# Optimization experiments

Hardware: AMD Instinct MI355X
Metric: run time of the kernel (lower is better)

## Reference

```python
import jax, jax.numpy as jnp
import numpy as np

# --- config (Qwen3-Next linear attention defaults) ---
B, S, H = 1, 256, 2048
NK, NV, DK, DV, K = 4, 32, 128, 128, 4
KEY_DIM = NK * DK          # 512
VAL_DIM = NV * DV          # 4096
CONV_DIM = 2 * KEY_DIM + VAL_DIM  # 5120
EPS = 1e-6


def setup_inputs() -> dict:
    key = jax.random.key(0)
    ks = jax.random.split(key, 8)
    rn = lambda k, shape, sc: jax.random.normal(k, shape, jnp.float32) * sc
    return {
        "hidden_states": jax.random.normal(ks[0], (B, S, H), jnp.float32),
        "w_qkvz": rn(ks[1], (2 * KEY_DIM + 2 * VAL_DIM, H), 0.02),  # in_proj_qkvz weight
        "w_ba": rn(ks[2], (2 * NV, H), 0.02),                        # in_proj_ba weight
        "w_out": rn(ks[3], (H, VAL_DIM), 0.02),                      # out_proj weight
        "conv_w": rn(ks[4], (CONV_DIM, 1, K), 0.1),                  # depthwise conv weight [C,1,K]
        "dt_bias": jnp.ones((NV,), jnp.float32),
        "A_log": jnp.zeros((NV,), jnp.float32),
        "norm_w": jnp.ones((DV,), jnp.float32),
    }


def reference(hidden_states, w_qkvz, w_ba, w_out, conv_w, dt_bias, A_log, norm_w):
    b, s, _ = hidden_states.shape
    # input projections (Linear without bias: x @ W.T)
    qkvz = hidden_states @ w_qkvz.T                      # [B,S,9216]
    ba = hidden_states @ w_ba.T                          # [B,S,64]
    q, k, v, z = jnp.split(qkvz, [KEY_DIM, 2 * KEY_DIM, 2 * KEY_DIM + VAL_DIM], axis=-1)
    beta, alpha = jnp.split(ba, 2, axis=-1)              # each [B,S,NV]

    # causal depthwise conv over concat(q,k,v), then silu
    qkv = jnp.concatenate([q, k, v], axis=-1).transpose(0, 2, 1)   # [B,C,S]
    qkv = jax.lax.conv_general_dilated(
        qkv, conv_w, window_strides=(1,), padding=[(K - 1, 0)],
        dimension_numbers=("NCH", "OIH", "NCH"), feature_group_count=CONV_DIM)
    qkv = jax.nn.silu(qkv).transpose(0, 2, 1)            # [B,S,C]
    q, k, v = jnp.split(qkv, [KEY_DIM, 2 * KEY_DIM], axis=-1)

    q = q.reshape(b, s, NK, DK)
    k = k.reshape(b, s, NK, DK)
    v = v.reshape(b, s, NV, DV)
    z = z.reshape(b, s, NV, DV)

    # GQA-style head expansion (repeat_interleave)
    ratio = NV // NK
    q = jnp.repeat(q, ratio, axis=2)                     # [B,S,NV,DK]
    k = jnp.repeat(k, ratio, axis=2)

    # NOTE: original computes g = -softplus(-A_log - alpha) but never uses it (dead code).
    beta_g = jax.nn.sigmoid(beta + dt_bias)[..., None]   # [B,S,NV,1]
    q = q * (DK ** -0.5)

    # naive delta-rule: full outer-product tensor + cumsum (memory-bound)
    kv = jnp.einsum("bsnk,bsnv->bsnkv", k, v * beta_g)   # [B,S,NV,DK,DV]
    out = jnp.einsum("bsnk,bsnkv->bsnv", q, jnp.cumsum(kv, axis=1))  # [B,S,NV,DV]

    # gated RMSNorm over head_v_dim in fp32
    of = out.astype(jnp.float32)
    var = jnp.mean(of * of, axis=-1, keepdims=True)
    of = of * jax.lax.rsqrt(var + EPS) * norm_w
    of = of * jax.nn.silu(z.astype(jnp.float32))

    return of.reshape(b, s, VAL_DIM) @ w_out.T           # [B,S,H]
```

## Files before the change

### kernel.cpp

```cpp
#include <hip/hip_runtime.h>
#include <hip/hip_bf16.h>

#define S_LEN   256
#define HID     2048
#define NVH     32
#define DKD     128
#define DVD     128
#define KEYDIM  512
#define VALDIM  4096
#define CONVDIM 5120
#define QKVZ_N  9216
#define EPS_F   1e-6f

typedef __attribute__((ext_vector_type(8))) short bf16x8;
typedef __attribute__((ext_vector_type(4))) float f32x4;

__device__ __forceinline__ unsigned short f2bf(float f) {
    union { float f; unsigned int i; } v; v.f = f;
    unsigned int x = v.i;
    return (unsigned short)((x + 0x7FFFu + ((x >> 16) & 1u)) >> 16);
}
__device__ __forceinline__ unsigned int pk2(float x, float y) {
    union { __hip_bfloat162 h; unsigned int u; } c;
    c.h = __float22bfloat162_rn(float2{x, y});
    return c.u;
}
__device__ __forceinline__ void gl_lds16(const void* g, void* l) {
    __builtin_amdgcn_global_load_lds(
        (const __attribute__((address_space(1))) unsigned int*)g,
        (__attribute__((address_space(3))) unsigned int*)l,
        16, 0, 0);
}

template<int NT>
__global__ __launch_bounds__(256, 3)
void gemm_db(const unsigned short* __restrict__ A, const float* __restrict__ B,
             float* __restrict__ Cpart, int N, int K, int kc) {
    __shared__ __align__(16) unsigned short As[2][128][64];
    __shared__ __align__(16) unsigned short Bs[2][NT][64];

    const int tid  = threadIdx.x;
    const int lane = tid & 63, wave = tid >> 6;
    const int wm = wave >> 1, wn = wave & 1;
    const int quad = lane >> 4, l16 = lane & 15;
    const int m0 = (blockIdx.x & 1) * 128;
    const int n0 = (blockIdx.x >> 1) * NT;
    const int kbeg = blockIdx.y * kc;
    const int niter = kc >> 6;

    const int a_ro = lane >> 3;
    const int a_gc = (lane & 7) ^ a_ro;

    const int rB = tid >> 2;
    const int cB = (tid & 3) * 16;
    const int swB = rB & 7;

    f32x4 acc[4][2];
#pragma unroll
    for (int i = 0; i < 4; i++)
#pragma unroll
        for (int j = 0; j < 2; j++) acc[i][j] = (f32x4){0.f, 0.f, 0.f, 0.f};

    float4 br[4];
    auto ldB = [&](int kk) {
        const float* p = B + (size_t)(n0 + rB) * K + kk + cB;
        br[0] = *(const float4*)(p);
        br[1] = *(const float4*)(p + 4);
        br[2] = *(const float4*)(p + 8);
        br[3] = *(const float4*)(p + 12);
    };
    auto wrB = [&](int buf) {
        uint4 u0, u1;
        u0.x = pk2(br[0].x, br[0].y); u0.y = pk2(br[0].z, br[0].w);
        u0.z = pk2(br[1].x, br[1].y); u0.w = pk2(br[1].z, br[1].w);
        u1.x = pk2(br[2].x, br[2].y); u1.y = pk2(br[2].z, br[2].w);
        u1.z = pk2(br[3].x, br[3].y); u1.w = pk2(br[3].z, br[3].w);
        int c0 = ((tid & 3) * 2) ^ swB;
        int c1 = ((tid & 3) * 2 + 1) ^ swB;
        *(uint4*)(&Bs[buf][rB][c0 * 8]) = u0;
        *(uint4*)(&Bs[buf][rB][c1 * 8]) = u1;
    };
    auto stageA = [&](int buf, int kk) {
#pragma unroll
        for (int t = 0; t < 4; ++t) {
            int rbase = wave * 32 + t * 8;
            gl_lds16(A + (size_t)(m0 + rbase + a_ro) * K + kk + a_gc * 8,
                     &As[buf][rbase][0]);
        }
    };
    auto compute = [&](int buf) {
#pragma unroll
        for (int ks = 0; ks < 2; ++ks) {
            bf16x8 af[4], bfr[2];
            int c = ((ks * 4 + quad) ^ (l16 & 7)) * 8;
#pragma unroll
            for (int i = 0; i < 4; ++i)
                af[i] = *(const bf16x8*)(&As[buf][wm * 64 + i * 16 + l16][c]);
#pragma unroll
            for (int j = 0; j < 2; ++j)
                bfr[j] = *(const bf16x8*)(&Bs[buf][wn * 32 + j * 16 + l16][c]);
#pragma unroll
            for (int i = 0; i < 4; ++i)
#pragma unroll
                for (int j = 0; j < 2; ++j)
                    acc[i][j] = __builtin_amdgcn_mfma_f32_16x16x32_bf16(af[i], bfr[j], acc[i][j], 0, 0, 0);
        }
    };

    ldB(kbeg);
    stageA(0, kbeg);
    wrB(0);
    if (niter > 1) ldB(kbeg + 64);
    __syncthreads();

    for (int it = 0; it < niter; ++it) {
        if (it + 1 < niter) stageA((it + 1) & 1, kbeg + (it + 1) * 64);
        compute(it & 1);
        if (it + 1 < niter) wrB((it + 1) & 1);
        if (it + 2 < niter) ldB(kbeg + (it + 2) * 64);
        __syncthreads();
    }

    float* C = Cpart + (size_t)blockIdx.y * 256 * N;
#pragma unroll
    for (int i = 0; i < 4; i++)
#pragma unroll
        for (int j = 0; j < 2; j++)
#pragma unroll
            for (int r = 0; r < 4; r++) {
                int row = m0 + wm * 64 + i * 16 + quad * 4 + r;
                int col = n0 + wn * 32 + j * 16 + l16;
                C[(size_t)row * N + col] = acc[i][j][r];
            }
}

template<int P>
__global__ void reduce_sum(const float* __restrict__ part, float* __restrict__ out, int n) {
    int i = (blockIdx.x * 256 + threadIdx.x) * 4;
    if (i >= n) return;
    float4 s = *(const float4*)(part + i);
#pragma unroll
    for (int p = 1; p < P; p++) {
        float4 v = *(const float4*)(part + (size_t)p * n + i);
        s.x += v.x; s.y += v.y; s.z += v.z; s.w += v.w;
    }
    *(float4*)(out + i) = s;
}

__global__ __launch_bounds__(256)
void ba_proj_cvt(const float* __restrict__ hs, const float* __restrict__ w_ba,
                 float* __restrict__ ba, unsigned short* __restrict__ abf) {
    int s = blockIdx.x;
    int n = threadIdx.x & 63, seg = threadIdx.x >> 6;
    const float* x = hs + (size_t)s * HID + seg * 512;
    const float* w = w_ba + (size_t)n * HID + seg * 512;
    float acc = 0.f;
#pragma unroll 4
    for (int k = 0; k < 512; k += 4) {
        float4 xv = *(const float4*)(x + k);
        float4 wv = *(const float4*)(w + k);
        acc += xv.x * wv.x + xv.y * wv.y + xv.z * wv.z + xv.w * wv.w;
    }
    __shared__ float parts[4][64];
    parts[seg][n] = acc;
    {
        int d = threadIdx.x * 8;
        const float4* p = (const float4*)(hs + (size_t)s * HID + d);
        float4 a = p[0], b = p[1];
        uint4 r;
        r.x = pk2(a.x, a.y); r.y = pk2(a.z, a.w);
        r.z = pk2(b.x, b.y); r.w = pk2(b.z, b.w);
        *(uint4*)(abf + (size_t)s * HID + d) = r;
    }
    __syncthreads();
    if (threadIdx.x < 64)
        ba[s * 64 + threadIdx.x] = parts[0][threadIdx.x] + parts[1][threadIdx.x]
                                 + parts[2][threadIdx.x] + parts[3][threadIdx.x];
}

template<int P>
__global__ __launch_bounds__(256)
void sum_conv(const float* __restrict__ part, const float* __restrict__ conv_w,
              float* __restrict__ conv, float* __restrict__ zs) {
    const int s0 = blockIdx.y * 8;
    const int c  = blockIdx.x * 1024 + threadIdx.x * 4;
    auto sum4 = [&](int s) {
        const float* p = part + (size_t)s * QKVZ_N + c;
        float4 v = *(const float4*)p;
#pragma unroll
        for (int q = 1; q < P; q++) {
            float4 w = *(const float4*)(p + (size_t)q * S_LEN * QKVZ_N);
            v.x += w.x; v.y += w.y; v.z += w.z; v.w += w.w;
        }
        return v;
    };
    if (c < CONVDIM) {
        float4 cw[4];
#pragma unroll
        for (int i = 0; i < 4; ++i) cw[i] = *(const float4*)(conv_w + (size_t)(c + i) * 4);
        float4 w0{0,0,0,0}, w1{0,0,0,0}, w2{0,0,0,0};
        for (int s = (s0 >= 3 ? s0 - 3 : 0); s < s0; ++s) { w0 = w1; w1 = w2; w2 = sum4(s); }
        for (int s = s0; s < s0 + 8; ++s) {
            float4 w3 = sum4(s);
            float4 o;
            o.x = w0.x * cw[0].x + w1.x * cw[0].y + w2.x * cw[0].z + w3.x * cw[0].w;
            o.y = w0.y * cw[1].x + w1.y * cw[1].y + w2.y * cw[1].z + w3.y * cw[1].w;
            o.z = w0.z * cw[2].x + w1.z * cw[2].y + w2.z * cw[2].z + w3.z * cw[2].w;
            o.w = w0.w * cw[3].x + w1.w * cw[3].y + w2.w * cw[3].z + w3.w * cw[3].w;
            o.x = o.x / (1.f + __expf(-o.x));
            o.y = o.y / (1.f + __expf(-o.y));
            o.z = o.z / (1.f + __expf(-o.z));
            o.w = o.w / (1.f + __expf(-o.w));
            *(float4*)(conv + (size_t)s * CONVDIM + c) = o;
            w0 = w1; w1 = w2; w2 = w3;
        }
    } else {
        for (int s = s0; s < s0 + 8; ++s) {
            float4 v = sum4(s);
            *(float4*)(zs + (size_t)s * VALDIM + (c - CONVDIM)) = v;
        }
    }
}

__global__ __launch_bounds__(256)
void scores_k(const float* __restrict__ conv, const float* __restrict__ ba,
              const float* __restrict__ dt_bias, float* __restrict__ scores) {
    int p = blockIdx.x;
    int st = (int)((__fsqrt_rn(8.f * p + 1.f) - 1.f) * 0.5f);
    while ((st + 1) * (st + 2) / 2 <= p) st++;
    while (st * (st + 1) / 2 > p) st--;
    int tt = p - st * (st + 1) / 2;
    int hk = blockIdx.y;
    int s0 = st * 16, t0 = tt * 16;
    __shared__ float Qs[16][132], Ks[16][132];
    int tid = threadIdx.x;
    int qoff = hk * DKD;
    int koff = KEYDIM + hk * DKD;
    for (int idx = tid; idx < 16 * 128; idx += 256) {
        int i = idx >> 7, d = idx & 127;
        Qs[i][d] = conv[(size_t)(s0 + i) * CONVDIM + qoff + d];
        Ks[i][d] = conv[(size_t)(t0 + i) * CONVDIM + koff + d];
    }
    __syncthreads();
    int tx = tid & 15, ty = tid >> 4;
    int s = s0 + ty, t = t0 + tx;
    float dot = 0.f;
    for (int d = 0; d < 128; d++) dot += Qs[ty][d] * Ks[tx][d];
    float base = (t <= s) ? dot * 0.08838834764831845f : 0.f;
#pragma unroll
    for (int v = 0; v < 8; v++) {
        int n = hk * 8 + v;
        float b = ba[t * 64 + n] + dt_bias[n];
        float bg = 1.f / (1.f + __expf(-b));
        scores[((size_t)n * 256 + s) * 256 + t] = base * bg;
    }
}

__global__ __launch_bounds__(256)
void attn_rms(const float* __restrict__ scores, const float* __restrict__ conv,
              const float* __restrict__ zs, const float* __restrict__ norm_w,
              unsigned short* __restrict__ normed) {
    int n = blockIdx.y, s0 = blockIdx.x * 16;
    int voff = 2 * KEYDIM + n * DVD;
    __shared__ float Ss[16][17];
    __shared__ float Vs[16][132];
    int tid = threadIdx.x, sy = tid >> 4, dx = tid & 15;
    float acc[8] = {0.f, 0.f, 0.f, 0.f, 0.f, 0.f, 0.f, 0.f};
    for (int t0 = 0; t0 <= s0; t0 += 16) {
        Ss[sy][dx] = scores[((size_t)n * 256 + s0 + sy) * 256 + t0 + dx];
        const float* vp = conv + (size_t)(t0 + sy) * CONVDIM + voff + dx * 8;
        *(float4*)&Vs[sy][dx * 8]     = *(const float4*)vp;
        *(float4*)&Vs[sy][dx * 8 + 4] = *(const float4*)(vp + 4);
        __syncthreads();
#pragma unroll
        for (int j = 0; j < 16; j++) {
            float sv = Ss[sy][j];
#pragma unroll
            for (int r = 0; r < 8; r++) acc[r] += sv * Vs[j][dx + 16 * r];
        }
        __syncthreads();
    }
    float ssq = 0.f;
#pragma unroll
    for (int r = 0; r < 8; r++) ssq += acc[r] * acc[r];
#pragma unroll
    for (int m = 1; m <= 8; m <<= 1) ssq += __shfl_xor(ssq, m, 64);
    float inv = rsqrtf(ssq * (1.f / 128.f) + EPS_F);
    int s = s0 + sy;
#pragma unroll
    for (int r = 0; r < 8; r++) {
        int d = dx + 16 * r;
        float z = zs[(size_t)s * VALDIM + n * DVD + d];
        float sz = z / (1.f + __expf(-z));
        float v = acc[r] * inv * norm_w[d] * sz;
        normed[((size_t)s * NVH + n) * DVD + d] = f2bf(v);
    }
}

extern "C" void kernel_launch(void* const* d_in, const int* in_sizes, int n_in,
                              void* d_out, int out_size, void* d_ws, size_t ws_size,
                              hipStream_t stream) {
    const float* hs      = (const float*)d_in[0];
    const float* w_qkvz  = (const float*)d_in[1];
    const float* w_ba    = (const float*)d_in[2];
    const float* w_out   = (const float*)d_in[3];
    const float* conv_w  = (const float*)d_in[4];
    const float* dt_bias = (const float*)d_in[5];
    const float* norm_w  = (const float*)d_in[7];

    char* ws = (char*)d_ws;
    unsigned short* abf = (unsigned short*)ws; ws += (size_t)S_LEN * HID * 2;
    float* ba   = (float*)ws;  ws += (size_t)S_LEN * 64 * 4;
    float* conv = (float*)ws;  ws += (size_t)S_LEN * CONVDIM * 4;
    float* zs   = (float*)ws;  ws += (size_t)S_LEN * VALDIM * 4;
    char* regB = ws;
    const bool big = ws_size >= (size_t)50 * 1024 * 1024;
    const int sk1 = big ? 4 : 2;
    const int sk2 = big ? 8 : 4;
    float* scratch1 = (float*)regB;
    unsigned short* normed = (unsigned short*)regB;
    float* scratch2 = (float*)(regB + 2097152);
    float* scores   = (float*)(regB + 2097152 + (size_t)sk2 * 2097152);

    ba_proj_cvt<<<S_LEN, 256, 0, stream>>>(hs, w_ba, ba, abf);
    gemm_db<64><<<dim3(2 * (QKVZ_N / 64), sk1), 256, 0, stream>>>(abf, w_qkvz, scratch1, QKVZ_N, HID, HID / sk1);
    if (big) sum_conv<4><<<dim3(9, 32), 256, 0, stream>>>(scratch1, conv_w, conv, zs);
    else     sum_conv<2><<<dim3(9, 32), 256, 0, stream>>>(scratch1, conv_w, conv, zs);
    scores_k<<<dim3(136, 4), 256, 0, stream>>>(conv, ba, dt_bias, scores);
    attn_rms<<<dim3(16, NVH), 256, 0, stream>>>(scores, conv, zs, norm_w, normed);
    gemm_db<64><<<dim3(2 * (HID / 64), sk2), 256, 0, stream>>>(normed, w_out, scratch2, HID, VALDIM, VALDIM / sk2);
    if (big) reduce_sum<8><<<(S_LEN * HID) / 1024, 256, 0, stream>>>(scratch2, (float*)d_out, S_LEN * HID);
    else     reduce_sum<4><<<(S_LEN * HID) / 1024, 256, 0, stream>>>(scratch2, (float*)d_out, S_LEN * HID);
}
```

Before: 247.0 us.

## Triple-buffer A in GEMM, drop split-K for QKVZ projection, read z directly

The GEMM now keeps A tiles in a three-stage LDS ring with two register sets for B, prefetching two iterations ahead. It uses a lighter barrier that waits only on LDS counters, with occupancy lowered from 3 to 2 blocks. The QKVZ projection no longer splits K, so the partial-sum reduction in the conv kernel and the separate z buffer go away; attn_rms reads z straight from the qkvz output. The out-projection split-K is fixed at 4 regardless of workspace size. This may under-fill the GPU for the first GEMM (288 blocks) in exchange for less memory traffic, and the barrier no longer waits on vmcnt, which relies on the global_load_lds ordering being correct.

```diff
diff --git a/kernel.cpp b/kernel.cpp
--- a/kernel.cpp
+++ b/kernel.cpp
@@ -31,12 +31,19 @@
         (__attribute__((address_space(3))) unsigned int*)l,
         16, 0, 0);
 }
+__device__ __forceinline__ void pipe_barrier() {
+    __builtin_amdgcn_sched_barrier(0);
+    asm volatile("s_waitcnt lgkmcnt(0)" ::: "memory");
+    __builtin_amdgcn_s_barrier();
+    asm volatile("" ::: "memory");
+    __builtin_amdgcn_sched_barrier(0);
+}
 
 template<int NT>
-__global__ __launch_bounds__(256, 3)
+__global__ __launch_bounds__(256, 2)
 void gemm_db(const unsigned short* __restrict__ A, const float* __restrict__ B,
              float* __restrict__ Cpart, int N, int K, int kc) {
-    __shared__ __align__(16) unsigned short As[2][128][64];
+    __shared__ __align__(16) unsigned short As[3][128][64];
     __shared__ __align__(16) unsigned short Bs[2][NT][64];
 
     const int tid  = threadIdx.x;
@@ -50,7 +57,6 @@
 
     const int a_ro = lane >> 3;
     const int a_gc = (lane & 7) ^ a_ro;
-
     const int rB = tid >> 2;
     const int cB = (tid & 3) * 16;
     const int swB = rB & 7;
@@ -61,15 +67,16 @@
 #pragma unroll
         for (int j = 0; j < 2; j++) acc[i][j] = (f32x4){0.f, 0.f, 0.f, 0.f};
 
-    float4 br[4];
-    auto ldB = [&](int kk) {
+    float4 brA[4], brB[4];
+
+    auto ldB = [&](float4 (&br)[4], int kk) {
         const float* p = B + (size_t)(n0 + rB) * K + kk + cB;
         br[0] = *(const float4*)(p);
         br[1] = *(const float4*)(p + 4);
         br[2] = *(const float4*)(p + 8);
         br[3] = *(const float4*)(p + 12);
     };
-    auto wrB = [&](int buf) {
+    auto wrB = [&](int bb, float4 (&br)[4]) {
         uint4 u0, u1;
         u0.x = pk2(br[0].x, br[0].y); u0.y = pk2(br[0].z, br[0].w);
         u0.z = pk2(br[1].x, br[1].y); u0.w = pk2(br[1].z, br[1].w);
@@ -77,28 +84,28 @@
         u1.z = pk2(br[3].x, br[3].y); u1.w = pk2(br[3].z, br[3].w);
         int c0 = ((tid & 3) * 2) ^ swB;
         int c1 = ((tid & 3) * 2 + 1) ^ swB;
-        *(uint4*)(&Bs[buf][rB][c0 * 8]) = u0;
-        *(uint4*)(&Bs[buf][rB][c1 * 8]) = u1;
-    };
-    auto stageA = [&](int buf, int kk) {
+        *(uint4*)(&Bs[bb][rB][c0 * 8]) = u0;
+        *(uint4*)(&Bs[bb][rB][c1 * 8]) = u1;
+    };
+    auto stageA = [&](int ab, int kk) {
 #pragma unroll
         for (int t = 0; t < 4; ++t) {
             int rbase = wave * 32 + t * 8;
             gl_lds16(A + (size_t)(m0 + rbase + a_ro) * K + kk + a_gc * 8,
-                     &As[buf][rbase][0]);
+                     &As[ab][rbase][0]);
         }
     };
-    auto compute = [&](int buf) {
+    auto compute = [&](int ab, int bb) {
 #pragma unroll
         for (int ks = 0; ks < 2; ++ks) {
             bf16x8 af[4], bfr[2];
             int c = ((ks * 4 + quad) ^ (l16 & 7)) * 8;
 #pragma unroll
             for (int i = 0; i < 4; ++i)
-                af[i] = *(const bf16x8*)(&As[buf][wm * 64 + i * 16 + l16][c]);
+                af[i] = *(const bf16x8*)(&As[ab][wm * 64 + i * 16 + l16][c]);
 #pragma unroll
             for (int j = 0; j < 2; ++j)
-                bfr[j] = *(const bf16x8*)(&Bs[buf][wn * 32 + j * 16 + l16][c]);
+                bfr[j] = *(const bf16x8*)(&Bs[bb][wn * 32 + j * 16 + l16][c]);
 #pragma unroll
             for (int i = 0; i < 4; ++i)
 #pragma unroll
@@ -107,18 +114,27 @@
         }
     };
 
-    ldB(kbeg);
+    auto step = [&](int it, float4 (&brLoad)[4], float4 (&brCons)[4]) {
+        if (it + 2 < niter) {
+            int kn = kbeg + (it + 2) * 64;
+            stageA((it + 2) % 3, kn);
+            ldB(brLoad, kn);
+        }
+        if (it + 1 < niter) wrB((it + 1) & 1, brCons);
+        compute(it % 3, it & 1);
+        pipe_barrier();
+    };
+
     stageA(0, kbeg);
-    wrB(0);
-    if (niter > 1) ldB(kbeg + 64);
-    __syncthreads();
-
-    for (int it = 0; it < niter; ++it) {
-        if (it + 1 < niter) stageA((it + 1) & 1, kbeg + (it + 1) * 64);
-        compute(it & 1);
-        if (it + 1 < niter) wrB((it + 1) & 1);
-        if (it + 2 < niter) ldB(kbeg + (it + 2) * 64);
-        __syncthreads();
+    ldB(brA, kbeg);
+    if (niter > 1) { stageA(1, kbeg + 64); ldB(brB, kbeg + 64); }
+    wrB(0, brA);
+    pipe_barrier();
+
+    int it = 0;
+    while (true) {
+        step(it, brA, brB); ++it; if (it >= niter) break;
+        step(it, brB, brA); ++it; if (it >= niter) break;
     }
 
     float* C = Cpart + (size_t)blockIdx.y * 256 * N;
@@ -178,47 +194,30 @@
                                  + parts[2][threadIdx.x] + parts[3][threadIdx.x];
 }
 
-template<int P>
 __global__ __launch_bounds__(256)
-void sum_conv(const float* __restrict__ part, const float* __restrict__ conv_w,
-              float* __restrict__ conv, float* __restrict__ zs) {
+void conv_silu4(const float* __restrict__ qkvz, const float* __restrict__ conv_w,
+                float* __restrict__ conv) {
     const int s0 = blockIdx.y * 8;
     const int c  = blockIdx.x * 1024 + threadIdx.x * 4;
-    auto sum4 = [&](int s) {
-        const float* p = part + (size_t)s * QKVZ_N + c;
-        float4 v = *(const float4*)p;
-#pragma unroll
-        for (int q = 1; q < P; q++) {
-            float4 w = *(const float4*)(p + (size_t)q * S_LEN * QKVZ_N);
-            v.x += w.x; v.y += w.y; v.z += w.z; v.w += w.w;
-        }
-        return v;
-    };
-    if (c < CONVDIM) {
-        float4 cw[4];
-#pragma unroll
-        for (int i = 0; i < 4; ++i) cw[i] = *(const float4*)(conv_w + (size_t)(c + i) * 4);
-        float4 w0{0,0,0,0}, w1{0,0,0,0}, w2{0,0,0,0};
-        for (int s = (s0 >= 3 ? s0 - 3 : 0); s < s0; ++s) { w0 = w1; w1 = w2; w2 = sum4(s); }
-        for (int s = s0; s < s0 + 8; ++s) {
-            float4 w3 = sum4(s);
-            float4 o;
-            o.x = w0.x * cw[0].x + w1.x * cw[0].y + w2.x * cw[0].z + w3.x * cw[0].w;
-            o.y = w0.y * cw[1].x + w1.y * cw[1].y + w2.y * cw[1].z + w3.y * cw[1].w;
-            o.z = w0.z * cw[2].x + w1.z * cw[2].y + w2.z * cw[2].z + w3.z * cw[2].w;
-            o.w = w0.w * cw[3].x + w1.w * cw[3].y + w2.w * cw[3].z + w3.w * cw[3].w;
-            o.x = o.x / (1.f + __expf(-o.x));
-            o.y = o.y / (1.f + __expf(-o.y));
-            o.z = o.z / (1.f + __expf(-o.z));
-            o.w = o.w / (1.f + __expf(-o.w));
-            *(float4*)(conv + (size_t)s * CONVDIM + c) = o;
-            w0 = w1; w1 = w2; w2 = w3;
-        }
-    } else {
-        for (int s = s0; s < s0 + 8; ++s) {
-            float4 v = sum4(s);
-            *(float4*)(zs + (size_t)s * VALDIM + (c - CONVDIM)) = v;
-        }
+    auto rd4 = [&](int s) { return *(const float4*)(qkvz + (size_t)s * QKVZ_N + c); };
+    float4 cw[4];
+#pragma unroll
+    for (int i = 0; i < 4; ++i) cw[i] = *(const float4*)(conv_w + (size_t)(c + i) * 4);
+    float4 w0{0,0,0,0}, w1{0,0,0,0}, w2{0,0,0,0};
+    for (int s = (s0 >= 3 ? s0 - 3 : 0); s < s0; ++s) { w0 = w1; w1 = w2; w2 = rd4(s); }
+    for (int s = s0; s < s0 + 8; ++s) {
+        float4 w3 = rd4(s);
+        float4 o;
+        o.x = w0.x * cw[0].x + w1.x * cw[0].y + w2.x * cw[0].z + w3.x * cw[0].w;
+        o.y = w0.y * cw[1].x + w1.y * cw[1].y + w2.y * cw[1].z + w3.y * cw[1].w;
+        o.z = w0.z * cw[2].x + w1.z * cw[2].y + w2.z * cw[2].z + w3.z * cw[2].w;
+        o.w = w0.w * cw[3].x + w1.w * cw[3].y + w2.w * cw[3].z + w3.w * cw[3].w;
+        o.x = o.x / (1.f + __expf(-o.x));
+        o.y = o.y / (1.f + __expf(-o.y));
+        o.z = o.z / (1.f + __expf(-o.z));
+        o.w = o.w / (1.f + __expf(-o.w));
+        *(float4*)(conv + (size_t)s * CONVDIM + c) = o;
+        w0 = w1; w1 = w2; w2 = w3;
     }
 }
 
@@ -258,7 +257,7 @@
 
 __global__ __launch_bounds__(256)
 void attn_rms(const float* __restrict__ scores, const float* __restrict__ conv,
-              const float* __restrict__ zs, const float* __restrict__ norm_w,
+              const float* __restrict__ qkvz, const float* __restrict__ norm_w,
               unsigned short* __restrict__ normed) {
     int n = blockIdx.y, s0 = blockIdx.x * 16;
     int voff = 2 * KEYDIM + n * DVD;
@@ -290,7 +289,7 @@
 #pragma unroll
     for (int r = 0; r < 8; r++) {
         int d = dx + 16 * r;
-        float z = zs[(size_t)s * VALDIM + n * DVD + d];
+        float z = qkvz[(size_t)s * QKVZ_N + CONVDIM + n * DVD + d];
         float sz = z / (1.f + __expf(-z));
         float v = acc[r] * inv * norm_w[d] * sz;
         normed[((size_t)s * NVH + n) * DVD + d] = f2bf(v);
@@ -310,25 +309,18 @@
 
     char* ws = (char*)d_ws;
     unsigned short* abf = (unsigned short*)ws; ws += (size_t)S_LEN * HID * 2;
-    float* ba   = (float*)ws;  ws += (size_t)S_LEN * 64 * 4;
-    float* conv = (float*)ws;  ws += (size_t)S_LEN * CONVDIM * 4;
-    float* zs   = (float*)ws;  ws += (size_t)S_LEN * VALDIM * 4;
-    char* regB = ws;
-    const bool big = ws_size >= (size_t)50 * 1024 * 1024;
-    const int sk1 = big ? 4 : 2;
-    const int sk2 = big ? 8 : 4;
-    float* scratch1 = (float*)regB;
-    unsigned short* normed = (unsigned short*)regB;
-    float* scratch2 = (float*)(regB + 2097152);
-    float* scores   = (float*)(regB + 2097152 + (size_t)sk2 * 2097152);
+    float* ba     = (float*)ws;  ws += (size_t)S_LEN * 64 * 4;
+    float* qkvz   = (float*)ws;  ws += (size_t)S_LEN * QKVZ_N * 4;
+    float* conv   = (float*)ws;  ws += (size_t)S_LEN * CONVDIM * 4;
+    unsigned short* normed = (unsigned short*)ws; ws += (size_t)S_LEN * VALDIM * 2;
+    float* scores = (float*)ws;  ws += (size_t)NVH * S_LEN * S_LEN * 4;
+    float* scratch2 = (float*)ws;
 
     ba_proj_cvt<<<S_LEN, 256, 0, stream>>>(hs, w_ba, ba, abf);
-    gemm_db<64><<<dim3(2 * (QKVZ_N / 64), sk1), 256, 0, stream>>>(abf, w_qkvz, scratch1, QKVZ_N, HID, HID / sk1);
-    if (big) sum_conv<4><<<dim3(9, 32), 256, 0, stream>>>(scratch1, conv_w, conv, zs);
-    else     sum_conv<2><<<dim3(9, 32), 256, 0, stream>>>(scratch1, conv_w, conv, zs);
+    gemm_db<64><<<dim3(2 * (QKVZ_N / 64), 1), 256, 0, stream>>>(abf, w_qkvz, qkvz, QKVZ_N, HID, HID);
+    conv_silu4<<<dim3(5, 32), 256, 0, stream>>>(qkvz, conv_w, conv);
     scores_k<<<dim3(136, 4), 256, 0, stream>>>(conv, ba, dt_bias, scores);
-    attn_rms<<<dim3(16, NVH), 256, 0, stream>>>(scores, conv, zs, norm_w, normed);
-    gemm_db<64><<<dim3(2 * (HID / 64), sk2), 256, 0, stream>>>(normed, w_out, scratch2, HID, VALDIM, VALDIM / sk2);
-    if (big) reduce_sum<8><<<(S_LEN * HID) / 1024, 256, 0, stream>>>(scratch2, (float*)d_out, S_LEN * HID);
-    else     reduce_sum<4><<<(S_LEN * HID) / 1024, 256, 0, stream>>>(scratch2, (float*)d_out, S_LEN * HID);
-}
+    attn_rms<<<dim3(16, NVH), 256, 0, stream>>>(scores, conv, qkvz, norm_w, normed);
+    gemm_db<64><<<dim3(2 * (HID / 64), 4), 256, 0, stream>>>(normed, w_out, scratch2, HID, VALDIM, VALDIM / 4);
+    reduce_sum<4><<<(S_LEN * HID) / 1024, 256, 0, stream>>>(scratch2, (float*)d_out, S_LEN * HID);
+}
```

Result: slower. 267.7 us (+8.4%).

## Deepen GEMM pipeline with triple-buffered A and ping-pong B register prefetch

Applied to the files above, without the earlier changes.

The bf16 GEMM kernel now keeps three LDS stages for A, filled by global_load_lds, and alternates two register sets for the fp32 B tiles. This gives a prefetch distance of two iterations, and the loop is manually unrolled to swap the register sets. The plain __syncthreads is replaced by a custom barrier with sched_barrier fences that waits only on lgkmcnt, so global loads stay in flight across the barrier. The aim is to hide global-memory latency better. In exchange, LDS use and register pressure rise and launch bounds drop from 3 to 2 waves per EU, and correctness depends on the compiler placing vmcnt waits correctly.

```diff
diff --git a/kernel.cpp b/kernel.cpp
--- a/kernel.cpp
+++ b/kernel.cpp
@@ -31,12 +31,19 @@
         (__attribute__((address_space(3))) unsigned int*)l,
         16, 0, 0);
 }
+__device__ __forceinline__ void pipe_barrier() {
+    __builtin_amdgcn_sched_barrier(0);
+    asm volatile("s_waitcnt lgkmcnt(0)" ::: "memory");
+    __builtin_amdgcn_s_barrier();
+    asm volatile("" ::: "memory");
+    __builtin_amdgcn_sched_barrier(0);
+}
 
 template<int NT>
-__global__ __launch_bounds__(256, 3)
+__global__ __launch_bounds__(256, 2)
 void gemm_db(const unsigned short* __restrict__ A, const float* __restrict__ B,
              float* __restrict__ Cpart, int N, int K, int kc) {
-    __shared__ __align__(16) unsigned short As[2][128][64];
+    __shared__ __align__(16) unsigned short As[3][128][64];
     __shared__ __align__(16) unsigned short Bs[2][NT][64];
 
     const int tid  = threadIdx.x;
@@ -50,7 +57,6 @@
 
     const int a_ro = lane >> 3;
     const int a_gc = (lane & 7) ^ a_ro;
-
     const int rB = tid >> 2;
     const int cB = (tid & 3) * 16;
     const int swB = rB & 7;
@@ -61,15 +67,16 @@
 #pragma unroll
         for (int j = 0; j < 2; j++) acc[i][j] = (f32x4){0.f, 0.f, 0.f, 0.f};
 
-    float4 br[4];
-    auto ldB = [&](int kk) {
+    float4 brA[4], brB[4];
+
+    auto ldB = [&](float4 (&br)[4], int kk) {
         const float* p = B + (size_t)(n0 + rB) * K + kk + cB;
         br[0] = *(const float4*)(p);
         br[1] = *(const float4*)(p + 4);
         br[2] = *(const float4*)(p + 8);
         br[3] = *(const float4*)(p + 12);
     };
-    auto wrB = [&](int buf) {
+    auto wrB = [&](int bb, float4 (&br)[4]) {
         uint4 u0, u1;
         u0.x = pk2(br[0].x, br[0].y); u0.y = pk2(br[0].z, br[0].w);
         u0.z = pk2(br[1].x, br[1].y); u0.w = pk2(br[1].z, br[1].w);
@@ -77,28 +84,28 @@
         u1.z = pk2(br[3].x, br[3].y); u1.w = pk2(br[3].z, br[3].w);
         int c0 = ((tid & 3) * 2) ^ swB;
         int c1 = ((tid & 3) * 2 + 1) ^ swB;
-        *(uint4*)(&Bs[buf][rB][c0 * 8]) = u0;
-        *(uint4*)(&Bs[buf][rB][c1 * 8]) = u1;
-    };
-    auto stageA = [&](int buf, int kk) {
+        *(uint4*)(&Bs[bb][rB][c0 * 8]) = u0;
+        *(uint4*)(&Bs[bb][rB][c1 * 8]) = u1;
+    };
+    auto stageA = [&](int ab, int kk) {
 #pragma unroll
         for (int t = 0; t < 4; ++t) {
             int rbase = wave * 32 + t * 8;
             gl_lds16(A + (size_t)(m0 + rbase + a_ro) * K + kk + a_gc * 8,
-                     &As[buf][rbase][0]);
-        }
-    };
-    auto compute = [&](int buf) {
+                     &As[ab][rbase][0]);
+        }
+    };
+    auto compute = [&](int ab, int bb) {
 #pragma unroll
         for (int ks = 0; ks < 2; ++ks) {
             bf16x8 af[4], bfr[2];
             int c = ((ks * 4 + quad) ^ (l16 & 7)) * 8;
 #pragma unroll
             for (int i = 0; i < 4; ++i)
-                af[i] = *(const bf16x8*)(&As[buf][wm * 64 + i * 16 + l16][c]);
+                af[i] = *(const bf16x8*)(&As[ab][wm * 64 + i * 16 + l16][c]);
 #pragma unroll
             for (int j = 0; j < 2; ++j)
-                bfr[j] = *(const bf16x8*)(&Bs[buf][wn * 32 + j * 16 + l16][c]);
+                bfr[j] = *(const bf16x8*)(&Bs[bb][wn * 32 + j * 16 + l16][c]);
 #pragma unroll
             for (int i = 0; i < 4; ++i)
 #pragma unroll
@@ -107,18 +114,27 @@
         }
     };
 
-    ldB(kbeg);
+    auto step = [&](int it, float4 (&brLoad)[4], float4 (&brCons)[4]) {
+        if (it + 2 < niter) {
+            int kn = kbeg + (it + 2) * 64;
+            stageA((it + 2) % 3, kn);
+            ldB(brLoad, kn);
+        }
+        if (it + 1 < niter) wrB((it + 1) & 1, brCons);
+        compute(it % 3, it & 1);
+        pipe_barrier();
+    };
+
     stageA(0, kbeg);
-    wrB(0);
-    if (niter > 1) ldB(kbeg + 64);
-    __syncthreads();
-
-    for (int it = 0; it < niter; ++it) {
-        if (it + 1 < niter) stageA((it + 1) & 1, kbeg + (it + 1) * 64);
-        compute(it & 1);
-        if (it + 1 < niter) wrB((it + 1) & 1);
-        if (it + 2 < niter) ldB(kbeg + (it + 2) * 64);
-        __syncthreads();
+    ldB(brA, kbeg);
+    if (niter > 1) { stageA(1, kbeg + 64); ldB(brB, kbeg + 64); }
+    wrB(0, brA);
+    pipe_barrier();
+
+    int it = 0;
+    while (true) {
+        step(it, brA, brB); ++it; if (it >= niter) break;
+        step(it, brB, brA); ++it; if (it >= niter) break;
     }
 
     float* C = Cpart + (size_t)blockIdx.y * 256 * N;
```

After: 260.7 us. +5.6%, slower.

## Replace LDS double-buffered GEMM with register-streaming GEMM and deeper split-K

Applied to the files above, without the earlier changes.

The shared-memory double-buffered GEMM is replaced by a kernel where each wave owns 16 output columns across all 256 rows. It streams fp32 weights straight into registers, converts them to bf16 and reads A fragments directly from global memory, with no LDS staging and no barriers. Split-K for the output projection goes up to 16/8 partitions, with a matching reduction and a higher workspace threshold. This targets the weight-bandwidth-bound GEMMs with a small M. The trade-off is heavy uncached A re-reads, more accumulator registers, and extra partial-sum traffic.

```diff
diff --git a/kernel.cpp b/kernel.cpp
--- a/kernel.cpp
+++ b/kernel.cpp
@@ -25,113 +25,48 @@
     c.h = __float22bfloat162_rn(float2{x, y});
     return c.u;
 }
-__device__ __forceinline__ void gl_lds16(const void* g, void* l) {
-    __builtin_amdgcn_global_load_lds(
-        (const __attribute__((address_space(1))) unsigned int*)g,
-        (__attribute__((address_space(3))) unsigned int*)l,
-        16, 0, 0);
-}
-
-template<int NT>
-__global__ __launch_bounds__(256, 3)
-void gemm_db(const unsigned short* __restrict__ A, const float* __restrict__ B,
-             float* __restrict__ Cpart, int N, int K, int kc) {
-    __shared__ __align__(16) unsigned short As[2][128][64];
-    __shared__ __align__(16) unsigned short Bs[2][NT][64];
-
+__device__ __forceinline__ bf16x8 pack_bf8(float4 lo, float4 hi) {
+    union { uint4 u; bf16x8 h; } c;
+    c.u.x = pk2(lo.x, lo.y); c.u.y = pk2(lo.z, lo.w);
+    c.u.z = pk2(hi.x, hi.y); c.u.w = pk2(hi.z, hi.w);
+    return c.h;
+}
+
+template<int KC>
+__global__ __launch_bounds__(256, 2)
+void gemm_stream(const unsigned short* __restrict__ A, const float* __restrict__ B,
+                 float* __restrict__ Cpart, int N, int K) {
     const int tid  = threadIdx.x;
     const int lane = tid & 63, wave = tid >> 6;
-    const int wm = wave >> 1, wn = wave & 1;
-    const int quad = lane >> 4, l16 = lane & 15;
-    const int m0 = (blockIdx.x & 1) * 128;
-    const int n0 = (blockIdx.x >> 1) * NT;
-    const int kbeg = blockIdx.y * kc;
-    const int niter = kc >> 6;
-
-    const int a_ro = lane >> 3;
-    const int a_gc = (lane & 7) ^ a_ro;
-
-    const int rB = tid >> 2;
-    const int cB = (tid & 3) * 16;
-    const int swB = rB & 7;
-
-    f32x4 acc[4][2];
-#pragma unroll
-    for (int i = 0; i < 4; i++)
-#pragma unroll
-        for (int j = 0; j < 2; j++) acc[i][j] = (f32x4){0.f, 0.f, 0.f, 0.f};
-
-    float4 br[4];
-    auto ldB = [&](int kk) {
-        const float* p = B + (size_t)(n0 + rB) * K + kk + cB;
-        br[0] = *(const float4*)(p);
-        br[1] = *(const float4*)(p + 4);
-        br[2] = *(const float4*)(p + 8);
-        br[3] = *(const float4*)(p + 12);
-    };
-    auto wrB = [&](int buf) {
-        uint4 u0, u1;
-        u0.x = pk2(br[0].x, br[0].y); u0.y = pk2(br[0].z, br[0].w);
-        u0.z = pk2(br[1].x, br[1].y); u0.w = pk2(br[1].z, br[1].w);
-        u1.x = pk2(br[2].x, br[2].y); u1.y = pk2(br[2].z, br[2].w);
-        u1.z = pk2(br[3].x, br[3].y); u1.w = pk2(br[3].z, br[3].w);
-        int c0 = ((tid & 3) * 2) ^ swB;
-        int c1 = ((tid & 3) * 2 + 1) ^ swB;
-        *(uint4*)(&Bs[buf][rB][c0 * 8]) = u0;
-        *(uint4*)(&Bs[buf][rB][c1 * 8]) = u1;
-    };
-    auto stageA = [&](int buf, int kk) {
-#pragma unroll
-        for (int t = 0; t < 4; ++t) {
-            int rbase = wave * 32 + t * 8;
-            gl_lds16(A + (size_t)(m0 + rbase + a_ro) * K + kk + a_gc * 8,
-                     &As[buf][rbase][0]);
-        }
-    };
-    auto compute = [&](int buf) {
-#pragma unroll
-        for (int ks = 0; ks < 2; ++ks) {
-            bf16x8 af[4], bfr[2];
-            int c = ((ks * 4 + quad) ^ (l16 & 7)) * 8;
-#pragma unroll
-            for (int i = 0; i < 4; ++i)
-                af[i] = *(const bf16x8*)(&As[buf][wm * 64 + i * 16 + l16][c]);
-#pragma unroll
-            for (int j = 0; j < 2; ++j)
-                bfr[j] = *(const bf16x8*)(&Bs[buf][wn * 32 + j * 16 + l16][c]);
-#pragma unroll
-            for (int i = 0; i < 4; ++i)
-#pragma unroll
-                for (int j = 0; j < 2; ++j)
-                    acc[i][j] = __builtin_amdgcn_mfma_f32_16x16x32_bf16(af[i], bfr[j], acc[i][j], 0, 0, 0);
-        }
-    };
-
-    ldB(kbeg);
-    stageA(0, kbeg);
-    wrB(0);
-    if (niter > 1) ldB(kbeg + 64);
-    __syncthreads();
-
-    for (int it = 0; it < niter; ++it) {
-        if (it + 1 < niter) stageA((it + 1) & 1, kbeg + (it + 1) * 64);
-        compute(it & 1);
-        if (it + 1 < niter) wrB((it + 1) & 1);
-        if (it + 2 < niter) ldB(kbeg + (it + 2) * 64);
-        __syncthreads();
-    }
-
-    float* C = Cpart + (size_t)blockIdx.y * 256 * N;
-#pragma unroll
-    for (int i = 0; i < 4; i++)
-#pragma unroll
-        for (int j = 0; j < 2; j++)
-#pragma unroll
-            for (int r = 0; r < 4; r++) {
-                int row = m0 + wm * 64 + i * 16 + quad * 4 + r;
-                int col = n0 + wn * 32 + j * 16 + l16;
-                C[(size_t)row * N + col] = acc[i][j][r];
-            }
+    const int l16 = lane & 15, quad = lane >> 4;
+    const int n0 = blockIdx.x * 64 + wave * 16;
+    const int kbeg = blockIdx.y * KC;
+
+    const unsigned short* a0 = A + (size_t)l16 * K + kbeg + quad * 8;
+    const float*          b0 = B + (size_t)(n0 + l16) * K + kbeg + quad * 8;
+
+    f32x4 acc[16];
+#pragma unroll
+    for (int i = 0; i < 16; i++) acc[i] = (f32x4){0.f, 0.f, 0.f, 0.f};
+
+#pragma unroll 4
+    for (int ks = 0; ks < KC; ks += 32) {
+        float4 x = *(const float4*)(b0 + ks);
+        float4 y = *(const float4*)(b0 + ks + 4);
+        bf16x8 bf = pack_bf8(x, y);
+#pragma unroll
+        for (int i = 0; i < 16; i++) {
+            bf16x8 af = *(const bf16x8*)(a0 + (size_t)i * 16 * K + ks);
+            acc[i] = __builtin_amdgcn_mfma_f32_16x16x32_bf16(af, bf, acc[i], 0, 0, 0);
+        }
+    }
+
+    float* C = Cpart + (size_t)blockIdx.y * 256 * N + n0 + l16;
+#pragma unroll
+    for (int i = 0; i < 16; i++)
+#pragma unroll
+        for (int r = 0; r < 4; r++)
+            C[(size_t)(i * 16 + quad * 4 + r) * N] = acc[i][r];
 }
 
 template<int P>
@@ -314,21 +249,23 @@
     float* conv = (float*)ws;  ws += (size_t)S_LEN * CONVDIM * 4;
     float* zs   = (float*)ws;  ws += (size_t)S_LEN * VALDIM * 4;
     char* regB = ws;
-    const bool big = ws_size >= (size_t)50 * 1024 * 1024;
+    const bool big = ws_size >= (size_t)60 * 1024 * 1024;
     const int sk1 = big ? 4 : 2;
-    const int sk2 = big ? 8 : 4;
+    const int sk2 = big ? 16 : 8;
     float* scratch1 = (float*)regB;
     unsigned short* normed = (unsigned short*)regB;
     float* scratch2 = (float*)(regB + 2097152);
     float* scores   = (float*)(regB + 2097152 + (size_t)sk2 * 2097152);
 
     ba_proj_cvt<<<S_LEN, 256, 0, stream>>>(hs, w_ba, ba, abf);
-    gemm_db<64><<<dim3(2 * (QKVZ_N / 64), sk1), 256, 0, stream>>>(abf, w_qkvz, scratch1, QKVZ_N, HID, HID / sk1);
+    if (big) gemm_stream<512> <<<dim3(QKVZ_N / 64, 4), 256, 0, stream>>>(abf, w_qkvz, scratch1, QKVZ_N, HID);
+    else     gemm_stream<1024><<<dim3(QKVZ_N / 64, 2), 256, 0, stream>>>(abf, w_qkvz, scratch1, QKVZ_N, HID);
     if (big) sum_conv<4><<<dim3(9, 32), 256, 0, stream>>>(scratch1, conv_w, conv, zs);
     else     sum_conv<2><<<dim3(9, 32), 256, 0, stream>>>(scratch1, conv_w, conv, zs);
     scores_k<<<dim3(136, 4), 256, 0, stream>>>(conv, ba, dt_bias, scores);
     attn_rms<<<dim3(16, NVH), 256, 0, stream>>>(scores, conv, zs, norm_w, normed);
-    gemm_db<64><<<dim3(2 * (HID / 64), sk2), 256, 0, stream>>>(normed, w_out, scratch2, HID, VALDIM, VALDIM / sk2);
-    if (big) reduce_sum<8><<<(S_LEN * HID) / 1024, 256, 0, stream>>>(scratch2, (float*)d_out, S_LEN * HID);
-    else     reduce_sum<4><<<(S_LEN * HID) / 1024, 256, 0, stream>>>(scratch2, (float*)d_out, S_LEN * HID);
-}
+    if (big) gemm_stream<256><<<dim3(HID / 64, 16), 256, 0, stream>>>(normed, w_out, scratch2, HID, VALDIM);
+    else     gemm_stream<512><<<dim3(HID / 64,  8), 256, 0, stream>>>(normed, w_out, scratch2, HID, VALDIM);
+    if (big) reduce_sum<16><<<(S_LEN * HID) / 1024, 256, 0, stream>>>(scratch2, (float*)d_out, S_LEN * HID);
+    else     reduce_sum<8> <<<(S_LEN * HID) / 1024, 256, 0, stream>>>(scratch2, (float*)d_out, S_LEN * HID);
+}
```

Result: slower. 342.6 us (+38.7%).
